# Kernel optimization log

Hardware: AMD Instinct MI355X
Metric: run time of the kernel (lower is better)

Reference implementation:

```python
import jax, jax.numpy as jnp
import numpy as np

# bitsandbytes NF4 codebook (16 levels, normalized to [-1, 1])
NF4_CODE = jnp.array([
    -1.0, -0.6961928009986877, -0.5250730514526367, -0.39491748809814453,
    -0.28444138169288635, -0.18477343022823334, -0.09105003625154495, 0.0,
    0.07958029955625534, 0.16093020141124725, 0.24611230194568634,
    0.33791524171829224, 0.44070982933044434, 0.5626170039176941,
    0.7229568362236023, 1.0], dtype=jnp.float32)

BLOCK = 64  # bitsandbytes default quantization blocksize
TOK, DIN, DOUT, RANK = 8192, 4096, 4096, 16
LORA_ALPHA = 16
SCALING = LORA_ALPHA / RANK ** 0.5  # rslora


def setup_inputs() -> dict:
    key = jax.random.key(0)
    k1, k2, k3, k4, k5, k6 = jax.random.split(key, 6)
    x = jax.random.normal(k1, (TOK, DIN), dtype=jnp.float32)
    w_codes = jax.random.randint(k2, (DOUT, DIN), 0, 16, dtype=jnp.int32)
    absmax = jax.random.uniform(k3, (DOUT, DIN // BLOCK), dtype=jnp.float32)
    bias = jax.random.normal(k4, (DOUT,), dtype=jnp.float32)
    lora_A = jax.random.normal(k5, (DIN, RANK), dtype=jnp.float32) * (1.0 / DIN ** 0.5)
    lora_B = jax.random.normal(k6, (RANK, DOUT), dtype=jnp.float32) * 0.02
    return {"x": x, "w_codes": w_codes, "absmax": absmax, "bias": bias,
            "lora_A": lora_A, "lora_B": lora_B}


def reference(x, w_codes, absmax, bias, lora_A, lora_B):
    # Dequantize NF4 base weight: codebook lookup * per-block absmax scale
    # W: [DOUT, DIN], absmax broadcast over blocks of 64 along DIN
    W = NF4_CODE[w_codes] * jnp.repeat(absmax, BLOCK, axis=1)
    base_out = x @ W.T + bias                      # [TOK, DOUT]
    lora_out = (x @ lora_A) @ lora_B               # low-rank path [TOK, DOUT]
    return base_out + lora_out * SCALING
```

## Files before the change

kernel.cpp:

```cpp
#include <hip/hip_runtime.h>
#include <hip/hip_bf16.h>
#include <cstdint>
#include <cstddef>

#define TOK   8192
#define DIN   4096
#define DOUT  4096
#define RANK  16
#define KE    4160
#define NKT64 (KE / 64)

#define BM 256
#define BN 256

#define PXB 512
#define DQB 8192
#define TLB 16

typedef __attribute__((ext_vector_type(8))) short bf16x8;
typedef __attribute__((ext_vector_type(4))) float f32x4;
typedef __attribute__((ext_vector_type(4))) int i32x4;
typedef __attribute__((ext_vector_type(8))) unsigned short u16x8;

__device__ __constant__ float NF4_CODE_D[16] = {
    -1.0f, -0.6961928009986877f, -0.5250730514526367f, -0.39491748809814453f,
    -0.28444138169288635f, -0.18477343022823334f, -0.09105003625154495f, 0.0f,
    0.07958029955625534f, 0.16093020141124725f, 0.24611230194568634f,
    0.33791524171829224f, 0.44070982933044434f, 0.5626170039176941f,
    0.7229568362236023f, 1.0f};

__device__ __forceinline__ unsigned short f2bf(float f) {
    union { float f; unsigned u; } v; v.f = f;
    unsigned u = v.u;
    unsigned r = (u + 0x7FFFu + ((u >> 16) & 1u)) >> 16;
    return (unsigned short)r;
}

__device__ __forceinline__ void async_copy16(const void* g, void* l) {
    __builtin_amdgcn_global_load_lds(
        (const __attribute__((address_space(1))) void*)g,
        (__attribute__((address_space(3))) void*)l,
        16, 0, 0);
}

__global__ __launch_bounds__(256) void prep_fused(
        const float* __restrict__ x, const float* __restrict__ lora_A,
        const int* __restrict__ codes, const float* __restrict__ absmax,
        const float* __restrict__ bias, const float* __restrict__ lora_B,
        unsigned short* __restrict__ xe, unsigned short* __restrict__ we) {
    __shared__ float tab[16];
    const int bid = blockIdx.x;
    const int tid = threadIdx.x;

    if (bid < PXB) {
        const int l = tid & 63;
        const int w = tid >> 6;
        const int t0 = bid * 16 + w * 4;

        float p[4][16];
#pragma unroll
        for (int a = 0; a < 4; ++a)
#pragma unroll
            for (int r = 0; r < 16; ++r) p[a][r] = 0.f;

        for (int it = 0; it < 8; ++it) {
            const int kb = it * 512 + l * 8;
            f32x4 xv[4][2];
#pragma unroll
            for (int a = 0; a < 4; ++a) {
                const f32x4* xp = (const f32x4*)(x + (size_t)(t0 + a) * DIN + kb);
                xv[a][0] = __builtin_nontemporal_load(xp);
                xv[a][1] = __builtin_nontemporal_load(xp + 1);
            }
#pragma unroll
            for (int a = 0; a < 4; ++a) {
                u16x8 s;
#pragma unroll
                for (int h = 0; h < 2; ++h) {
                    s[h * 4 + 0] = f2bf(xv[a][h].x);
                    s[h * 4 + 1] = f2bf(xv[a][h].y);
                    s[h * 4 + 2] = f2bf(xv[a][h].z);
                    s[h * 4 + 3] = f2bf(xv[a][h].w);
                }
                *(u16x8*)(xe + (size_t)(t0 + a) * KE + kb) = s;
            }
#pragma unroll
            for (int j = 0; j < 8; ++j) {
                const float4* ap = (const float4*)(lora_A + (size_t)(kb + j) * RANK);
                const float4 a0 = ap[0], a1 = ap[1], a2 = ap[2], a3 = ap[3];
                const float av[16] = {a0.x, a0.y, a0.z, a0.w, a1.x, a1.y, a1.z, a1.w,
                                      a2.x, a2.y, a2.z, a2.w, a3.x, a3.y, a3.z, a3.w};
#pragma unroll
                for (int a = 0; a < 4; ++a) {
                    const f32x4 xh = xv[a][j >> 2];
                    const float xs = (j & 3) == 0 ? xh.x : (j & 3) == 1 ? xh.y
                                   : (j & 3) == 2 ? xh.z : xh.w;
#pragma unroll
                    for (int r = 0; r < 16; ++r) p[a][r] += xs * av[r];
                }
            }
        }

#pragma unroll
        for (int a = 0; a < 4; ++a) {
#pragma unroll
            for (int r = 0; r < 16; ++r) {
                float v = p[a][r];
#pragma unroll
                for (int off = 32; off > 0; off >>= 1) v += __shfl_xor(v, off, 64);
                if (l == r)
                    xe[(size_t)(t0 + a) * KE + DIN + r] = f2bf(4.0f * v);
            }
            if (l >= 16)
                xe[(size_t)(t0 + a) * KE + DIN + l] =
                    (l == 16) ? (unsigned short)0x3F80u : (unsigned short)0u;
        }
    } else if (bid < PXB + DQB) {
        if (tid < 16) tab[tid] = NF4_CODE_D[tid];
        __syncthreads();
        const size_t t = (size_t)(bid - PXB) * 256 + tid;
        const size_t base = t * 8;
        const int o = (int)(base >> 12);
        const int k = (int)(base & (DIN - 1));
        const float am = absmax[base >> 6];
        const i32x4 c0 = __builtin_nontemporal_load((const i32x4*)(codes + base));
        const i32x4 c1 = __builtin_nontemporal_load((const i32x4*)(codes + base + 4));
        u16x8 ov;
        ov[0] = f2bf(tab[c0.x] * am);
        ov[1] = f2bf(tab[c0.y] * am);
        ov[2] = f2bf(tab[c0.z] * am);
        ov[3] = f2bf(tab[c0.w] * am);
        ov[4] = f2bf(tab[c1.x] * am);
        ov[5] = f2bf(tab[c1.y] * am);
        ov[6] = f2bf(tab[c1.z] * am);
        ov[7] = f2bf(tab[c1.w] * am);
        *(u16x8*)(we + (size_t)o * KE + k) = ov;
    } else {
        const int o = (bid - PXB - DQB) * 256 + tid;
        unsigned short* dst = we + (size_t)o * KE + DIN;
#pragma unroll
        for (int r = 0; r < RANK; ++r) dst[r] = f2bf(lora_B[(size_t)r * DOUT + o]);
        dst[16] = f2bf(bias[o]);
#pragma unroll
        for (int r = 17; r < 64; ++r) dst[r] = 0;
    }
}

__global__ __launch_bounds__(512, 2) void gemm_bt(const unsigned short* __restrict__ A,
                                                  const unsigned short* __restrict__ B,
                                                  float* __restrict__ C) {
    __shared__ __attribute__((aligned(1024))) char smem[4 * 32768];

    const int tid = threadIdx.x;
    const int l = tid & 63;
    const int w = tid >> 6;
    const int wm = w >> 2;
    const int wn = w & 3;

    const int tm = blockIdx.x >> 4;
    const int tn = blockIdx.x & 15;
    const int rowBase = tm * BM;
    const int colBase = tn * BN;

    int srow[2], scolb[2], loffs[2];
#pragma unroll
    for (int g = 0; g < 2; ++g) {
        const int loff = g * 8192 + tid * 16;
        const int soff = loff ^ (((loff >> 7) & 7) << 4);
        loffs[g] = loff;
        srow[g] = soff >> 6;
        scolb[g] = soff & 63;
    }

    auto stageA = [&](int tt, int kh, int slot) {
        char* dst = smem + slot * 32768;
        const int k0 = tt * 64 + kh * 32;
#pragma unroll
        for (int g = 0; g < 2; ++g)
            async_copy16((const char*)A + ((size_t)(rowBase + srow[g]) * KE + k0) * 2 + scolb[g],
                         dst + loffs[g]);
    };
    auto stageB = [&](int tt, int kh, int slot) {
        char* dst = smem + slot * 32768 + 16384;
        const int k0 = tt * 64 + kh * 32;
#pragma unroll
        for (int g = 0; g < 2; ++g)
            async_copy16((const char*)B + ((size_t)(colBase + srow[g]) * KE + k0) * 2 + scolb[g],
                         dst + loffs[g]);
    };

    const int lmask = ((l >> 1) & 7) << 4;
    const int aoff = (((wm * 128 + (l & 15)) * 64) + ((l >> 4) * 16)) ^ lmask;
    const int boff = (((wn * 64 + (l & 15)) * 64) + ((l >> 4) * 16)) ^ lmask;

    f32x4 acc[8][4];
#pragma unroll
    for (int m = 0; m < 8; ++m)
#pragma unroll
        for (int n = 0; n < 4; ++n) acc[m][n] = (f32x4){0.f, 0.f, 0.f, 0.f};

    bf16x8 aLo[4], aHi[4], aLo2[4], aHi2[4], bCur[4], bNxt[4];

    stageA(0, 0, 0); stageB(0, 0, 0);
    stageA(0, 1, 1); stageB(0, 1, 1);
    stageA(1, 0, 2); stageB(1, 0, 2);
    asm volatile("s_waitcnt vmcnt(8)" ::: "memory");
    __builtin_amdgcn_s_barrier();
    {
        const char* S0 = smem;
#pragma unroll
        for (int n = 0; n < 4; ++n)
            bCur[n] = *(const bf16x8*)(S0 + 16384 + boff + n * 1024);
#pragma unroll
        for (int m = 0; m < 4; ++m)
            aLo[m] = *(const bf16x8*)(S0 + aoff + m * 1024);
    }

    for (int t = 0; t < NKT64; ++t) {
        const char* S0 = smem + ((2 * t) & 3) * 32768;
        const char* S1 = smem + ((2 * t + 1) & 3) * 32768;
        const char* Sn = smem + ((2 * t + 2) & 3) * 32768;
        const int d1 = (2 * t + 3) & 3;
        const int e0 = (2 * t + 4) & 3;
        const bool more = (t + 1 < NKT64);
        const bool more2 = (t + 2 < NKT64);

#pragma unroll
        for (int m = 0; m < 4; ++m)
            aHi[m] = *(const bf16x8*)(S0 + aoff + (4 + m) * 1024);
        if (more) stageA(t + 1, 1, d1);
        __builtin_amdgcn_sched_barrier(0);
        __builtin_amdgcn_s_setprio(1);
#pragma unroll
        for (int m = 0; m < 4; ++m)
#pragma unroll
            for (int n = 0; n < 4; ++n)
                acc[m][n] = __builtin_amdgcn_mfma_f32_16x16x32_bf16(
                    aLo[m], bCur[n], acc[m][n], 0, 0, 0);
        __builtin_amdgcn_s_setprio(0);
        __builtin_amdgcn_sched_barrier(0);

        if (more) {
            asm volatile("s_waitcnt vmcnt(6)" ::: "memory");
        } else {
            asm volatile("s_waitcnt vmcnt(0)" ::: "memory");
        }
        __builtin_amdgcn_s_barrier();
        __builtin_amdgcn_sched_barrier(0);
#pragma unroll
        for (int n = 0; n < 4; ++n)
            bNxt[n] = *(const bf16x8*)(S1 + 16384 + boff + n * 1024);
#pragma unroll
        for (int m = 0; m < 4; ++m)
            aLo2[m] = *(const bf16x8*)(S1 + aoff + m * 1024);
        if (more) stageB(t + 1, 1, d1);
        __builtin_amdgcn_sched_barrier(0);
        __builtin_amdgcn_s_setprio(1);
#pragma unroll
        for (int m = 0; m < 4; ++m)
#pragma unroll
            for (int n = 0; n < 4; ++n)
                acc[4 + m][n] = __builtin_amdgcn_mfma_f32_16x16x32_bf16(
                    aHi[m], bCur[n], acc[4 + m][n], 0, 0, 0);
        __builtin_amdgcn_s_setprio(0);
        __builtin_amdgcn_sched_barrier(0);

#pragma unroll
        for (int m = 0; m < 4; ++m)
            aHi2[m] = *(const bf16x8*)(S1 + aoff + (4 + m) * 1024);
        if (more2) stageA(t + 2, 0, e0);
        __builtin_amdgcn_sched_barrier(0);
        __builtin_amdgcn_s_setprio(1);
#pragma unroll
        for (int m = 0; m < 4; ++m)
#pragma unroll
            for (int n = 0; n < 4; ++n)
                acc[m][n] = __builtin_amdgcn_mfma_f32_16x16x32_bf16(
                    aLo2[m], bNxt[n], acc[m][n], 0, 0, 0);
        __builtin_amdgcn_s_setprio(0);
        __builtin_amdgcn_sched_barrier(0);

        if (more) {
            asm volatile("s_waitcnt vmcnt(4)" ::: "memory");
            __builtin_amdgcn_s_barrier();
            __builtin_amdgcn_sched_barrier(0);
#pragma unroll
            for (int n = 0; n < 4; ++n)
                bCur[n] = *(const bf16x8*)(Sn + 16384 + boff + n * 1024);
#pragma unroll
            for (int m = 0; m < 4; ++m)
                aLo[m] = *(const bf16x8*)(Sn + aoff + m * 1024);
            if (more2) stageB(t + 2, 0, e0);
        }
        __builtin_amdgcn_sched_barrier(0);
        __builtin_amdgcn_s_setprio(1);
#pragma unroll
        for (int m = 0; m < 4; ++m)
#pragma unroll
            for (int n = 0; n < 4; ++n)
                acc[4 + m][n] = __builtin_amdgcn_mfma_f32_16x16x32_bf16(
                    aHi2[m], bNxt[n], acc[4 + m][n], 0, 0, 0);
        __builtin_amdgcn_s_setprio(0);
        __builtin_amdgcn_sched_barrier(0);
    }

#pragma unroll
    for (int m = 0; m < 8; ++m) {
        const int rowg = rowBase + wm * 128 + m * 16 + (l >> 4) * 4;
#pragma unroll
        for (int n = 0; n < 4; ++n) {
            const int colg = colBase + wn * 64 + n * 16 + (l & 15);
            float* cp = C + (size_t)rowg * DOUT + colg;
#pragma unroll
            for (int r = 0; r < 4; ++r) cp[(size_t)r * DOUT] = acc[m][n][r];
        }
    }
}

extern "C" void kernel_launch(void* const* d_in, const int* in_sizes, int n_in,
                              void* d_out, int out_size, void* d_ws, size_t ws_size,
                              hipStream_t stream) {
    const float* x      = (const float*)d_in[0];
    const int*   codes  = (const int*)d_in[1];
    const float* absmax = (const float*)d_in[2];
    const float* bias   = (const float*)d_in[3];
    const float* lora_A = (const float*)d_in[4];
    const float* lora_B = (const float*)d_in[5];
    float* out = (float*)d_out;

    unsigned short* xe = (unsigned short*)d_ws;
    unsigned short* we = xe + (size_t)TOK * KE;

    prep_fused<<<PXB + DQB + TLB, 256, 0, stream>>>(x, lora_A, codes, absmax,
                                                    bias, lora_B, xe, we);
    gemm_bt<<<(TOK / BM) * (DOUT / BN), 512, 0, stream>>>(xe, we, out);
}
```

Before: 360.9 us.

## Shrink GEMM tile to 256x128 with 4 waves and triple-buffered LDS

```diff
diff --git a/kernel.cpp b/kernel.cpp
--- a/kernel.cpp
+++ b/kernel.cpp
@@ -11,7 +11,7 @@
 #define NKT64 (KE / 64)
 
 #define BM 256
-#define BN 256
+#define BN 128
 
 #define PXB 512
 #define DQB 8192
@@ -146,52 +146,56 @@
     }
 }
 
-__global__ __launch_bounds__(512, 2) void gemm_bt(const unsigned short* __restrict__ A,
+__global__ __launch_bounds__(256, 2) void gemm_bt(const unsigned short* __restrict__ A,
                                                   const unsigned short* __restrict__ B,
                                                   float* __restrict__ C) {
-    __shared__ __attribute__((aligned(1024))) char smem[4 * 32768];
+    __shared__ __attribute__((aligned(1024))) char smem[3 * 24576];
 
     const int tid = threadIdx.x;
     const int l = tid & 63;
     const int w = tid >> 6;
-    const int wm = w >> 2;
-    const int wn = w & 3;
-
-    const int tm = blockIdx.x >> 4;
-    const int tn = blockIdx.x & 15;
+    const int wm = w >> 1;
+    const int wn = w & 1;
+
+    const int tm = blockIdx.x >> 5;
+    const int tn = blockIdx.x & 31;
     const int rowBase = tm * BM;
     const int colBase = tn * BN;
 
-    int srow[2], scolb[2], loffs[2];
+    int aRow[4], aCol[4], bRow[2], bCol[2];
+#pragma unroll
+    for (int g = 0; g < 4; ++g) {
+        const int loff = g * 4096 + tid * 16;
+        const int soff = loff ^ (((loff >> 7) & 7) << 4);
+        aRow[g] = soff >> 6; aCol[g] = soff & 63;
+    }
 #pragma unroll
     for (int g = 0; g < 2; ++g) {
-        const int loff = g * 8192 + tid * 16;
+        const int loff = g * 4096 + tid * 16;
         const int soff = loff ^ (((loff >> 7) & 7) << 4);
-        loffs[g] = loff;
-        srow[g] = soff >> 6;
-        scolb[g] = soff & 63;
+        bRow[g] = soff >> 6; bCol[g] = soff & 63;
     }
 
     auto stageA = [&](int tt, int kh, int slot) {
-        char* dst = smem + slot * 32768;
+        char* dst = smem + slot * 24576;
         const int k0 = tt * 64 + kh * 32;
 #pragma unroll
-        for (int g = 0; g < 2; ++g)
-            async_copy16((const char*)A + ((size_t)(rowBase + srow[g]) * KE + k0) * 2 + scolb[g],
-                         dst + loffs[g]);
+        for (int g = 0; g < 4; ++g)
+            async_copy16((const char*)A + ((size_t)(rowBase + aRow[g]) * KE + k0) * 2 + aCol[g],
+                         dst + g * 4096 + tid * 16);
     };
     auto stageB = [&](int tt, int kh, int slot) {
-        char* dst = smem + slot * 32768 + 16384;
+        char* dst = smem + slot * 24576 + 16384;
         const int k0 = tt * 64 + kh * 32;
 #pragma unroll
         for (int g = 0; g < 2; ++g)
-            async_copy16((const char*)B + ((size_t)(colBase + srow[g]) * KE + k0) * 2 + scolb[g],
-                         dst + loffs[g]);
+            async_copy16((const char*)B + ((size_t)(colBase + bRow[g]) * KE + k0) * 2 + bCol[g],
+                         dst + g * 4096 + tid * 16);
     };
 
     const int lmask = ((l >> 1) & 7) << 4;
     const int aoff = (((wm * 128 + (l & 15)) * 64) + ((l >> 4) * 16)) ^ lmask;
-    const int boff = (((wn * 64 + (l & 15)) * 64) + ((l >> 4) * 16)) ^ lmask;
+    const int boff = 16384 + ((((wn * 64 + (l & 15)) * 64) + ((l >> 4) * 16)) ^ lmask);
 
     f32x4 acc[8][4];
 #pragma unroll
@@ -203,32 +207,32 @@
 
     stageA(0, 0, 0); stageB(0, 0, 0);
     stageA(0, 1, 1); stageB(0, 1, 1);
-    stageA(1, 0, 2); stageB(1, 0, 2);
-    asm volatile("s_waitcnt vmcnt(8)" ::: "memory");
+    asm volatile("s_waitcnt vmcnt(6)" ::: "memory");
     __builtin_amdgcn_s_barrier();
     {
         const char* S0 = smem;
 #pragma unroll
         for (int n = 0; n < 4; ++n)
-            bCur[n] = *(const bf16x8*)(S0 + 16384 + boff + n * 1024);
+            bCur[n] = *(const bf16x8*)(S0 + boff + n * 1024);
 #pragma unroll
         for (int m = 0; m < 4; ++m)
             aLo[m] = *(const bf16x8*)(S0 + aoff + m * 1024);
     }
 
     for (int t = 0; t < NKT64; ++t) {
-        const char* S0 = smem + ((2 * t) & 3) * 32768;
-        const char* S1 = smem + ((2 * t + 1) & 3) * 32768;
-        const char* Sn = smem + ((2 * t + 2) & 3) * 32768;
-        const int d1 = (2 * t + 3) & 3;
-        const int e0 = (2 * t + 4) & 3;
+        const int s0 = (2 * t) % 3;
+        const int s1 = (s0 + 1 == 3) ? 0 : s0 + 1;
+        const int sn = (s1 + 1 == 3) ? 0 : s1 + 1;
+        const int d1 = s0;
+        const char* S0 = smem + s0 * 24576;
+        const char* S1 = smem + s1 * 24576;
+        const char* Sn = smem + sn * 24576;
         const bool more = (t + 1 < NKT64);
-        const bool more2 = (t + 2 < NKT64);
 
 #pragma unroll
         for (int m = 0; m < 4; ++m)
             aHi[m] = *(const bf16x8*)(S0 + aoff + (4 + m) * 1024);
-        if (more) stageA(t + 1, 1, d1);
+        if (more) stageA(t + 1, 0, sn);
         __builtin_amdgcn_sched_barrier(0);
         __builtin_amdgcn_s_setprio(1);
 #pragma unroll
@@ -241,7 +245,7 @@
         __builtin_amdgcn_sched_barrier(0);
 
         if (more) {
-            asm volatile("s_waitcnt vmcnt(6)" ::: "memory");
+            asm volatile("s_waitcnt vmcnt(4)" ::: "memory");
         } else {
             asm volatile("s_waitcnt vmcnt(0)" ::: "memory");
         }
@@ -249,11 +253,11 @@
         __builtin_amdgcn_sched_barrier(0);
 #pragma unroll
         for (int n = 0; n < 4; ++n)
-            bNxt[n] = *(const bf16x8*)(S1 + 16384 + boff + n * 1024);
+            bNxt[n] = *(const bf16x8*)(S1 + boff + n * 1024);
 #pragma unroll
         for (int m = 0; m < 4; ++m)
             aLo2[m] = *(const bf16x8*)(S1 + aoff + m * 1024);
-        if (more) stageB(t + 1, 1, d1);
+        if (more) stageB(t + 1, 0, sn);
         __builtin_amdgcn_sched_barrier(0);
         __builtin_amdgcn_s_setprio(1);
 #pragma unroll
@@ -268,7 +272,7 @@
 #pragma unroll
         for (int m = 0; m < 4; ++m)
             aHi2[m] = *(const bf16x8*)(S1 + aoff + (4 + m) * 1024);
-        if (more2) stageA(t + 2, 0, e0);
+        if (more) stageA(t + 1, 1, d1);
         __builtin_amdgcn_sched_barrier(0);
         __builtin_amdgcn_s_setprio(1);
 #pragma unroll
@@ -286,11 +290,11 @@
             __builtin_amdgcn_sched_barrier(0);
 #pragma unroll
             for (int n = 0; n < 4; ++n)
-                bCur[n] = *(const bf16x8*)(Sn + 16384 + boff + n * 1024);
+                bCur[n] = *(const bf16x8*)(Sn + boff + n * 1024);
 #pragma unroll
             for (int m = 0; m < 4; ++m)
                 aLo[m] = *(const bf16x8*)(Sn + aoff + m * 1024);
-            if (more2) stageB(t + 2, 0, e0);
+            stageB(t + 1, 1, d1);
         }
         __builtin_amdgcn_sched_barrier(0);
         __builtin_amdgcn_s_setprio(1);
@@ -333,5 +337,5 @@
 
     prep_fused<<<PXB + DQB + TLB, 256, 0, stream>>>(x, lora_A, codes, absmax,
                                                     bias, lora_B, xe, we);
-    gemm_bt<<<(TOK / BM) * (DOUT / BN), 512, 0, stream>>>(xe, we, out);
-}
+    gemm_bt<<<(TOK / BM) * (DOUT / BN), 256, 0, stream>>>(xe, we, out);
+}
```

After: 394.9 us. +9.4%, slower.
